# Kernel tuning notes

Measured on AMD Instinct MI355X. Metric: run time of the kernel, lower is better.

The kernel has to match this reference:

```python
import jax, jax.numpy as jnp
import numpy as np
import math

EMBED_DIM = 1024
NUM_HEADS = 16
HEAD_DIM = EMBED_DIM // NUM_HEADS
SEQ = 1024
BATCH = 8


def setup_inputs() -> dict:
    key = jax.random.key(0)
    k1, k2, k3, k4, k5 = jax.random.split(key, 5)
    q = jax.random.normal(k1, (SEQ, BATCH, EMBED_DIM), dtype=jnp.float32)
    # module asserts key == query (self-attention only)
    in_proj_w = jax.random.normal(k2, (3 * EMBED_DIM, EMBED_DIM), dtype=jnp.float32) * 0.02
    in_proj_b = jax.random.normal(k3, (3 * EMBED_DIM,), dtype=jnp.float32) * 0.02
    out_proj_w = jax.random.normal(k4, (EMBED_DIM, EMBED_DIM), dtype=jnp.float32) * 0.02
    out_proj_b = jax.random.normal(k5, (EMBED_DIM,), dtype=jnp.float32) * 0.02
    return {
        "query": q,
        "key": q,
        "value": q,
        "in_proj_w": in_proj_w,
        "in_proj_b": in_proj_b,
        "out_proj_w": out_proj_w,
        "out_proj_b": out_proj_b,
    }


def reference(query, key, value, in_proj_w, in_proj_b, out_proj_w, out_proj_b):
    s, b, e = query.shape
    nh, hd = NUM_HEADS, HEAD_DIM
    norm = math.sqrt(hd)
    # fused QKV projection: [s, b, 3e]
    mixed = query @ in_proj_w.T + in_proj_b
    mixed = mixed.reshape(s, b, nh, 3 * hd)
    q, k, v = jnp.split(mixed, 3, axis=-1)  # each [s, b, nh, hd]
    # -> [b*nh, s, hd]
    q = q.reshape(s, b * nh, hd).transpose(1, 0, 2) / norm
    k = k.reshape(s, b * nh, hd).transpose(1, 0, 2)
    v = v.reshape(s, b * nh, hd).transpose(1, 0, 2)
    # full O(s^2) attention matrix, as in the original bmm/softmax/bmm
    scores = jnp.einsum('nqd,nkd->nqk', q, k)  # [b*nh, s, s]
    probs = jax.nn.softmax(scores, axis=-1)
    ctx = jnp.einsum('nqk,nkd->nqd', probs, v)  # [b*nh, s, hd]
    # [b*nh, s, hd] -> [s, b, e]
    ctx = ctx.reshape(b, nh, s, hd).transpose(2, 0, 1, 3).reshape(s, b, e)
    return ctx @ out_proj_w.T + out_proj_b
```

## Files before the change

### kernel.cpp

```cpp
#include <hip/hip_runtime.h>

typedef __bf16 bf16_t;
typedef __bf16 bf16x8 __attribute__((ext_vector_type(8)));
typedef float f32x4 __attribute__((ext_vector_type(4)));

#define MFMA16(a, b, c) __builtin_amdgcn_mfma_f32_16x16x32_bf16((a), (b), (c), 0, 0, 0)

__device__ __forceinline__ const bf16_t* tile_ptr(const bf16_t* t, int row, int kchunk) {
    return t + row * 64 + (((kchunk ^ (row & 7))) << 3);
}

__device__ __forceinline__ void stage64(const bf16_t* __restrict__ gbase, size_t gstride,
                                        bf16_t* lds_rowbase, int lane) {
    const int rr = lane >> 3, cl = lane & 7;
    const bf16_t* g = gbase + (size_t)rr * gstride + ((cl ^ rr) << 3);
    __builtin_amdgcn_global_load_lds((__attribute__((address_space(1))) const void*)g,
                                     (__attribute__((address_space(3))) void*)lds_rowbase,
                                     16, 0, 0);
}

__global__ void __launch_bounds__(256) k_cvt(
    const float* __restrict__ q, const float* __restrict__ wi, const float* __restrict__ wo,
    bf16_t* __restrict__ qb, bf16_t* __restrict__ wib, bf16_t* __restrict__ wob)
{
    const int g = blockIdx.x * 256 + threadIdx.x;
    const float* src; bf16_t* dst; int off;
    if (g < 1048576)      { src = q;  dst = qb;  off = g; }
    else if (g < 1441792) { src = wi; dst = wib; off = g - 1048576; }
    else                  { src = wo; dst = wob; off = g - 1441792; }
    const float4* s4 = (const float4*)(src + (size_t)off * 8);
    float4 a = s4[0], b = s4[1];
    bf16x8 v;
    v[0] = (bf16_t)a.x; v[1] = (bf16_t)a.y; v[2] = (bf16_t)a.z; v[3] = (bf16_t)a.w;
    v[4] = (bf16_t)b.x; v[5] = (bf16_t)b.y; v[6] = (bf16_t)b.z; v[7] = (bf16_t)b.w;
    *(bf16x8*)(dst + (size_t)off * 8) = v;
}

__global__ void __launch_bounds__(256) k_qkv(
    const bf16_t* __restrict__ A, const bf16_t* __restrict__ W,
    const float* __restrict__ bias,
    bf16_t* __restrict__ Qh, bf16_t* __restrict__ Kh, bf16_t* __restrict__ Vt)
{
    __shared__ bf16_t As[128 * 64];
    __shared__ bf16_t Bs[128 * 64];
    const int m0 = blockIdx.x * 128;
    const int n0 = blockIdx.y * 128;
    const int t = threadIdx.x;
    const int wave = t >> 6, lane = t & 63;
    const int quad = lane >> 4, l16 = lane & 15;
    const int wm = (wave & 1) * 64, wn = (wave >> 1) * 64;

    f32x4 acc[4][4] = {};

    for (int k0 = 0; k0 < 1024; k0 += 64) {
        __syncthreads();
        #pragma unroll
        for (int p = 0; p < 4; ++p) {
            const int rb = wave * 32 + p * 8;
            stage64(A + (size_t)(m0 + rb) * 1024 + k0, 1024, As + rb * 64, lane);
            stage64(W + (size_t)(n0 + rb) * 1024 + k0, 1024, Bs + rb * 64, lane);
        }
        __syncthreads();
        #pragma unroll
        for (int ks = 0; ks < 2; ++ks) {
            bf16x8 af[4], bf[4];
            #pragma unroll
            for (int i = 0; i < 4; ++i)
                af[i] = *(const bf16x8*)tile_ptr(As, wm + i * 16 + l16, ks * 4 + quad);
            #pragma unroll
            for (int j = 0; j < 4; ++j)
                bf[j] = *(const bf16x8*)tile_ptr(Bs, wn + j * 16 + l16, ks * 4 + quad);
            #pragma unroll
            for (int i = 0; i < 4; ++i)
                #pragma unroll
                for (int j = 0; j < 4; ++j)
                    acc[i][j] = MFMA16(af[i], bf[j], acc[i][j]);
        }
    }

    #pragma unroll
    for (int j = 0; j < 4; ++j) {
        const int n = n0 + wn + j * 16 + l16;
        const int h = n / 192;
        const int c = n - h * 192;
        const float bv = bias[n];
        #pragma unroll
        for (int i = 0; i < 4; ++i) {
            #pragma unroll
            for (int rg = 0; rg < 4; ++rg) {
                const int m = m0 + wm + i * 16 + quad * 4 + rg;
                const int si = m >> 3, bi = m & 7;
                const int head = bi * 16 + h;
                const float val = acc[i][j][rg] + bv;
                if (c < 64)
                    Qh[((size_t)head * 1024 + si) * 64 + c] = (bf16_t)(val * 0.125f);
                else if (c < 128)
                    Kh[((size_t)head * 1024 + si) * 64 + (c - 64)] = (bf16_t)val;
                else
                    Vt[((size_t)head * 64 + (c - 128)) * 1024 + si] = (bf16_t)val;
            }
        }
    }
}

__global__ void __launch_bounds__(256) k_attn(
    const bf16_t* __restrict__ Qh, const bf16_t* __restrict__ Kh,
    const bf16_t* __restrict__ Vg, bf16_t* __restrict__ Ctx)
{
    __shared__ bf16_t Qs[128 * 64];
    __shared__ bf16_t Ks[64 * 64];
    __shared__ bf16_t Vts[80 * 64];
    __shared__ bf16_t Ps[4][32][72];

    const int head = blockIdx.x >> 3;
    const int qt = blockIdx.x & 7;
    const int t = threadIdx.x;
    const int wave = t >> 6, lane = t & 63;
    const int quad = lane >> 4, l16 = lane & 15;

    const bf16_t* Qg = Qh + (size_t)head * 65536 + (size_t)qt * 8192;
    const bf16_t* Kg = Kh + (size_t)head * 65536;
    const bf16_t* Vgh = Vg + (size_t)head * 65536;

    #pragma unroll
    for (int p = 0; p < 4; ++p) {
        const int rb = wave * 32 + p * 8;
        stage64(Qg + (size_t)rb * 64, 64, Qs + rb * 64, lane);
    }
    #pragma unroll
    for (int i = 0; i < 4; ++i) {
        const int idx = t * 4 + i;
        Vts[64 * 64 + idx] = (bf16_t)((idx < 64) ? 1.0f : 0.0f);
    }
    __syncthreads();

    bf16x8 qf[2][2];
    #pragma unroll
    for (int half = 0; half < 2; ++half)
        #pragma unroll
        for (int ks = 0; ks < 2; ++ks)
            qf[half][ks] = *(const bf16x8*)tile_ptr(Qs, wave * 32 + half * 16 + l16, ks * 4 + quad);

    f32x4 vacc[2][5] = {};

    for (int kt = 0; kt < 16; ++kt) {
        __syncthreads();
        #pragma unroll
        for (int p = 0; p < 2; ++p) {
            const int rb = wave * 16 + p * 8;
            stage64(Kg + (size_t)(kt * 64 + rb) * 64, 64, Ks + rb * 64, lane);
            stage64(Vgh + (size_t)rb * 1024 + kt * 64, 1024, Vts + rb * 64, lane);
        }
        __syncthreads();

        f32x4 s[2][4] = {};
        #pragma unroll
        for (int ks = 0; ks < 2; ++ks) {
            #pragma unroll
            for (int j = 0; j < 4; ++j) {
                bf16x8 kf = *(const bf16x8*)tile_ptr(Ks, j * 16 + l16, ks * 4 + quad);
                s[0][j] = MFMA16(qf[0][ks], kf, s[0][j]);
                s[1][j] = MFMA16(qf[1][ks], kf, s[1][j]);
            }
        }

        #pragma unroll
        for (int half = 0; half < 2; ++half)
            #pragma unroll
            for (int j = 0; j < 4; ++j)
                #pragma unroll
                for (int rg = 0; rg < 4; ++rg)
                    Ps[wave][half * 16 + quad * 4 + rg][j * 16 + l16] =
                        (bf16_t)exp2f(s[half][j][rg] * 1.44269504088896f);
        asm volatile("s_waitcnt lgkmcnt(0)" ::: "memory");

        #pragma unroll
        for (int ks = 0; ks < 2; ++ks) {
            bf16x8 pf0 = *(const bf16x8*)&Ps[wave][l16][ks * 32 + quad * 8];
            bf16x8 pf1 = *(const bf16x8*)&Ps[wave][16 + l16][ks * 32 + quad * 8];
            #pragma unroll
            for (int n = 0; n < 5; ++n) {
                bf16x8 vf = *(const bf16x8*)tile_ptr(Vts, n * 16 + l16, ks * 4 + quad);
                vacc[0][n] = MFMA16(pf0, vf, vacc[0][n]);
                vacc[1][n] = MFMA16(pf1, vf, vacc[1][n]);
            }
        }
    }

    const int bi = head >> 4, h = head & 15;
    #pragma unroll
    for (int half = 0; half < 2; ++half) {
        #pragma unroll
        for (int rg = 0; rg < 4; ++rg) {
            const float l = __shfl(vacc[half][4][rg], lane & 48, 64);
            const float inv = 1.0f / l;
            const int si = qt * 128 + wave * 32 + half * 16 + quad * 4 + rg;
            #pragma unroll
            for (int n = 0; n < 4; ++n)
                Ctx[((size_t)si * 8 + bi) * 1024 + h * 64 + n * 16 + l16] =
                    (bf16_t)(vacc[half][n][rg] * inv);
        }
    }
}

__global__ void __launch_bounds__(256) k_out(
    const bf16_t* __restrict__ A, const bf16_t* __restrict__ W,
    const float* __restrict__ bias, float* __restrict__ out)
{
    __shared__ bf16_t As[128 * 64];
    __shared__ bf16_t Bs[128 * 64];
    const int m0 = blockIdx.x * 128;
    const int n0 = blockIdx.y * 128;
    const int t = threadIdx.x;
    const int wave = t >> 6, lane = t & 63;
    const int quad = lane >> 4, l16 = lane & 15;
    const int wm = (wave & 1) * 64, wn = (wave >> 1) * 64;

    f32x4 acc[4][4] = {};

    for (int k0 = 0; k0 < 1024; k0 += 64) {
        __syncthreads();
        #pragma unroll
        for (int p = 0; p < 4; ++p) {
            const int rb = wave * 32 + p * 8;
            stage64(A + (size_t)(m0 + rb) * 1024 + k0, 1024, As + rb * 64, lane);
            stage64(W + (size_t)(n0 + rb) * 1024 + k0, 1024, Bs + rb * 64, lane);
        }
        __syncthreads();
        #pragma unroll
        for (int ks = 0; ks < 2; ++ks) {
            bf16x8 af[4], bf[4];
            #pragma unroll
            for (int i = 0; i < 4; ++i)
                af[i] = *(const bf16x8*)tile_ptr(As, wm + i * 16 + l16, ks * 4 + quad);
            #pragma unroll
            for (int j = 0; j < 4; ++j)
                bf[j] = *(const bf16x8*)tile_ptr(Bs, wn + j * 16 + l16, ks * 4 + quad);
            #pragma unroll
            for (int i = 0; i < 4; ++i)
                #pragma unroll
                for (int j = 0; j < 4; ++j)
                    acc[i][j] = MFMA16(af[i], bf[j], acc[i][j]);
        }
    }

    #pragma unroll
    for (int j = 0; j < 4; ++j) {
        const int n = n0 + wn + j * 16 + l16;
        const float bv = bias[n];
        #pragma unroll
        for (int i = 0; i < 4; ++i) {
            #pragma unroll
            for (int rg = 0; rg < 4; ++rg) {
                const int m = m0 + wm + i * 16 + quad * 4 + rg;
                out[(size_t)m * 1024 + n] = acc[i][j][rg] + bv;
            }
        }
    }
}

extern "C" void kernel_launch(void* const* d_in, const int* in_sizes, int n_in,
                              void* d_out, int out_size, void* d_ws, size_t ws_size,
                              hipStream_t stream)
{
    const float* query = (const float*)d_in[0];
    const float* in_w  = (const float*)d_in[3];
    const float* in_b  = (const float*)d_in[4];
    const float* out_w = (const float*)d_in[5];
    const float* out_b = (const float*)d_in[6];
    float* out = (float*)d_out;

    bf16_t* Wi  = (bf16_t*)d_ws;
    bf16_t* Wo  = Wi + (size_t)3145728;
    bf16_t* Qh  = Wo + (size_t)1048576;
    bf16_t* Kh  = Qh + (size_t)8388608;
    bf16_t* Vt  = Kh + (size_t)8388608;
    bf16_t* Aq  = Vt + (size_t)8388608;
    bf16_t* Ctx = Aq;

    k_cvt<<<dim3(6144), 256, 0, stream>>>(query, in_w, out_w, Aq, Wi, Wo);
    k_qkv<<<dim3(64, 24), 256, 0, stream>>>(Aq, Wi, in_b, Qh, Kh, Vt);
    k_attn<<<dim3(1024), 256, 0, stream>>>(Qh, Kh, Vt, Ctx);
    k_out<<<dim3(64, 8), 256, 0, stream>>>(Ctx, Wo, out_b, out);
}
```

Baseline: 317.3 us.

## Stage QKV epilogue through LDS for coalesced stores and blocked V layout

The QKV GEMM now permutes weight rows so each 128-wide output tile is all Q, all K, or all V for two heads. The epilogue writes results into swizzled shared memory, then emits 16-byte coalesced stores instead of scattered 2-byte writes. V is stored in a blocked layout of 8-sequence chunks that the attention kernel loads directly. The attention kernel also keeps the ones column for the row-sum MFMA in registers instead of reading it from LDS. This adds an extra LDS round trip and index arithmetic in the epilogue.

```diff
diff --git a/kernel.cpp b/kernel.cpp
--- a/kernel.cpp
+++ b/kernel.cpp
@@ -17,6 +17,10 @@
     __builtin_amdgcn_global_load_lds((__attribute__((address_space(1))) const void*)g,
                                      (__attribute__((address_space(3))) void*)lds_rowbase,
                                      16, 0, 0);
+}
+
+__device__ __forceinline__ int cs_addr(int m, int n) {
+    return m * 128 + ((((n >> 3) ^ ((m >> 3) & 7))) << 3) + (n & 7);
 }
 
 __global__ void __launch_bounds__(256) k_cvt(
@@ -41,6 +45,221 @@
     const float* __restrict__ bias,
     bf16_t* __restrict__ Qh, bf16_t* __restrict__ Kh, bf16_t* __restrict__ Vt)
 {
+    __shared__ bf16_t smem[16384];
+    bf16_t* As = smem;
+    bf16_t* Bs = smem + 8192;
+    const int m0 = blockIdx.x * 128;
+    const int n0 = blockIdx.y * 128;
+    const int which = n0 >> 10;
+    const int hbase = (n0 & 1023) >> 6;
+    const int t = threadIdx.x;
+    const int wave = t >> 6, lane = t & 63;
+    const int quad = lane >> 4, l16 = lane & 15;
+    const int wm = (wave & 1) * 64, wn = (wave >> 1) * 64;
+
+    f32x4 acc[4][4] = {};
+
+    for (int k0 = 0; k0 < 1024; k0 += 64) {
+        __syncthreads();
+        #pragma unroll
+        for (int p = 0; p < 4; ++p) {
+            const int rb = wave * 32 + p * 8;
+            stage64(A + (size_t)(m0 + rb) * 1024 + k0, 1024, As + rb * 64, lane);
+            const int np = n0 + rb;
+            const int wrow = ((np & 1023) >> 6) * 192 + which * 64 + (np & 63);
+            stage64(W + (size_t)wrow * 1024 + k0, 1024, Bs + rb * 64, lane);
+        }
+        __syncthreads();
+        #pragma unroll
+        for (int ks = 0; ks < 2; ++ks) {
+            bf16x8 af[4], bf[4];
+            #pragma unroll
+            for (int i = 0; i < 4; ++i)
+                af[i] = *(const bf16x8*)tile_ptr(As, wm + i * 16 + l16, ks * 4 + quad);
+            #pragma unroll
+            for (int j = 0; j < 4; ++j)
+                bf[j] = *(const bf16x8*)tile_ptr(Bs, wn + j * 16 + l16, ks * 4 + quad);
+            #pragma unroll
+            for (int i = 0; i < 4; ++i)
+                #pragma unroll
+                for (int j = 0; j < 4; ++j)
+                    acc[i][j] = MFMA16(af[i], bf[j], acc[i][j]);
+        }
+    }
+
+    __syncthreads();
+    const float scale = (which == 0) ? 0.125f : 1.0f;
+    #pragma unroll
+    for (int j = 0; j < 4; ++j) {
+        const int nl = wn + j * 16 + l16;
+        const float bv = bias[(hbase + (nl >> 6)) * 192 + which * 64 + (nl & 63)];
+        #pragma unroll
+        for (int i = 0; i < 4; ++i) {
+            #pragma unroll
+            for (int rg = 0; rg < 4; ++rg) {
+                const int ml = wm + i * 16 + quad * 4 + rg;
+                smem[cs_addr(ml, nl)] = (bf16_t)((acc[i][j][rg] + bv) * scale);
+            }
+        }
+    }
+    __syncthreads();
+
+    const int si0 = m0 >> 3;
+    if (which < 2) {
+        bf16_t* dst = which ? Kh : Qh;
+        #pragma unroll
+        for (int u = 0; u < 4; ++u) {
+            const int unit = wave * 4 + u;
+            const int h = unit >> 3, bi = unit & 7;
+            const int head = bi * 16 + hbase + h;
+            #pragma unroll
+            for (int pass = 0; pass < 2; ++pass) {
+                const int si = pass * 8 + (lane >> 3);
+                const int dc = lane & 7;
+                const int ml = si * 8 + bi;
+                const int nch = (h * 8 + dc) ^ (si & 7);
+                bf16x8 v = *(const bf16x8*)&smem[ml * 128 + nch * 8];
+                *(bf16x8*)(dst + (size_t)head * 65536 + (size_t)(si0 + si) * 64 + dc * 8) = v;
+            }
+        }
+    } else {
+        #pragma unroll
+        for (int u = 0; u < 8; ++u) {
+            const int unit = wave * 8 + u;
+            const int h = unit >> 4, bi = (unit >> 1) & 7, c = unit & 1;
+            const int head = bi * 16 + hbase + h;
+            const int d = lane;
+            bf16x8 v;
+            #pragma unroll
+            for (int e = 0; e < 8; ++e) {
+                const int ml = (c * 8 + e) * 8 + bi;
+                const int nch = (h * 8 + (d >> 3)) ^ e;
+                v[e] = smem[ml * 128 + nch * 8 + (d & 7)];
+            }
+            *(bf16x8*)(Vt + (size_t)head * 65536 +
+                       (size_t)(si0 / 8 + c) * 512 + (size_t)d * 8) = v;
+        }
+    }
+}
+
+__global__ void __launch_bounds__(256) k_attn(
+    const bf16_t* __restrict__ Qh, const bf16_t* __restrict__ Kh,
+    const bf16_t* __restrict__ Vg, bf16_t* __restrict__ Ctx)
+{
+    __shared__ bf16_t Qs[128 * 64];
+    __shared__ bf16_t Ks[64 * 64];
+    __shared__ bf16_t Vts[80 * 64];
+    __shared__ bf16_t Ps[4][32][72];
+
+    const int head = blockIdx.x >> 3;
+    const int qt = blockIdx.x & 7;
+    const int t = threadIdx.x;
+    const int wave = t >> 6, lane = t & 63;
+    const int quad = lane >> 4, l16 = lane & 15;
+
+    const bf16_t* Qg = Qh + (size_t)head * 65536 + (size_t)qt * 8192;
+    const bf16_t* Kg = Kh + (size_t)head * 65536;
+    const bf16_t* Vgh = Vg + (size_t)head * 65536;
+
+    #pragma unroll
+    for (int p = 0; p < 4; ++p) {
+        const int rb = wave * 32 + p * 8;
+        stage64(Qg + (size_t)rb * 64, 64, Qs + rb * 64, lane);
+    }
+    #pragma unroll
+    for (int i = 0; i < 4; ++i) {
+        const int idx = t * 4 + i;
+        Vts[64 * 64 + idx] = (bf16_t)((idx < 64) ? 1.0f : 0.0f);
+    }
+    __syncthreads();
+
+    bf16x8 qf[2][2];
+    #pragma unroll
+    for (int half = 0; half < 2; ++half)
+        #pragma unroll
+        for (int ks = 0; ks < 2; ++ks)
+            qf[half][ks] = *(const bf16x8*)tile_ptr(Qs, wave * 32 + half * 16 + l16, ks * 4 + quad);
+
+    bf16x8 vf_ones[2];
+    #pragma unroll
+    for (int ks = 0; ks < 2; ++ks)
+        vf_ones[ks] = *(const bf16x8*)tile_ptr(Vts, 64 + l16, ks * 4 + quad);
+
+    f32x4 vacc[2][5] = {};
+
+    for (int kt = 0; kt < 16; ++kt) {
+        __syncthreads();
+        #pragma unroll
+        for (int p = 0; p < 2; ++p) {
+            const int rb = wave * 16 + p * 8;
+            stage64(Kg + (size_t)(kt * 64 + rb) * 64, 64, Ks + rb * 64, lane);
+            {
+                const int rr = lane >> 3, cl = lane & 7;
+                const bf16_t* g = Vgh + (size_t)(kt * 8 + (cl ^ rr)) * 512
+                                      + (size_t)(rb + rr) * 8;
+                __builtin_amdgcn_global_load_lds(
+                    (__attribute__((address_space(1))) const void*)g,
+                    (__attribute__((address_space(3))) void*)(Vts + rb * 64), 16, 0, 0);
+            }
+        }
+        __syncthreads();
+
+        f32x4 s[2][4] = {};
+        #pragma unroll
+        for (int ks = 0; ks < 2; ++ks) {
+            #pragma unroll
+            for (int j = 0; j < 4; ++j) {
+                bf16x8 kf = *(const bf16x8*)tile_ptr(Ks, j * 16 + l16, ks * 4 + quad);
+                s[0][j] = MFMA16(qf[0][ks], kf, s[0][j]);
+                s[1][j] = MFMA16(qf[1][ks], kf, s[1][j]);
+            }
+        }
+
+        #pragma unroll
+        for (int half = 0; half < 2; ++half)
+            #pragma unroll
+            for (int j = 0; j < 4; ++j)
+                #pragma unroll
+                for (int rg = 0; rg < 4; ++rg)
+                    Ps[wave][half * 16 + quad * 4 + rg][j * 16 + l16] =
+                        (bf16_t)exp2f(s[half][j][rg] * 1.44269504088896f);
+        asm volatile("s_waitcnt lgkmcnt(0)" ::: "memory");
+
+        #pragma unroll
+        for (int ks = 0; ks < 2; ++ks) {
+            bf16x8 pf0 = *(const bf16x8*)&Ps[wave][l16][ks * 32 + quad * 8];
+            bf16x8 pf1 = *(const bf16x8*)&Ps[wave][16 + l16][ks * 32 + quad * 8];
+            #pragma unroll
+            for (int n = 0; n < 4; ++n) {
+                bf16x8 vf = *(const bf16x8*)tile_ptr(Vts, n * 16 + l16, ks * 4 + quad);
+                vacc[0][n] = MFMA16(pf0, vf, vacc[0][n]);
+                vacc[1][n] = MFMA16(pf1, vf, vacc[1][n]);
+            }
+            vacc[0][4] = MFMA16(pf0, vf_ones[ks], vacc[0][4]);
+            vacc[1][4] = MFMA16(pf1, vf_ones[ks], vacc[1][4]);
+        }
+    }
+
+    const int bi = head >> 4, h = head & 15;
+    #pragma unroll
+    for (int half = 0; half < 2; ++half) {
+        #pragma unroll
+        for (int rg = 0; rg < 4; ++rg) {
+            const float l = __shfl(vacc[half][4][rg], lane & 48, 64);
+            const float inv = 1.0f / l;
+            const int si = qt * 128 + wave * 32 + half * 16 + quad * 4 + rg;
+            #pragma unroll
+            for (int n = 0; n < 4; ++n)
+                Ctx[((size_t)si * 8 + bi) * 1024 + h * 64 + n * 16 + l16] =
+                    (bf16_t)(vacc[half][n][rg] * inv);
+        }
+    }
+}
+
+__global__ void __launch_bounds__(256) k_out(
+    const bf16_t* __restrict__ A, const bf16_t* __restrict__ W,
+    const float* __restrict__ bias, float* __restrict__ out)
+{
     __shared__ bf16_t As[128 * 64];
     __shared__ bf16_t Bs[128 * 64];
     const int m0 = blockIdx.x * 128;
@@ -81,172 +300,6 @@
     #pragma unroll
     for (int j = 0; j < 4; ++j) {
         const int n = n0 + wn + j * 16 + l16;
-        const int h = n / 192;
-        const int c = n - h * 192;
-        const float bv = bias[n];
-        #pragma unroll
-        for (int i = 0; i < 4; ++i) {
-            #pragma unroll
-            for (int rg = 0; rg < 4; ++rg) {
-                const int m = m0 + wm + i * 16 + quad * 4 + rg;
-                const int si = m >> 3, bi = m & 7;
-                const int head = bi * 16 + h;
-                const float val = acc[i][j][rg] + bv;
-                if (c < 64)
-                    Qh[((size_t)head * 1024 + si) * 64 + c] = (bf16_t)(val * 0.125f);
-                else if (c < 128)
-                    Kh[((size_t)head * 1024 + si) * 64 + (c - 64)] = (bf16_t)val;
-                else
-                    Vt[((size_t)head * 64 + (c - 128)) * 1024 + si] = (bf16_t)val;
-            }
-        }
-    }
-}
-
-__global__ void __launch_bounds__(256) k_attn(
-    const bf16_t* __restrict__ Qh, const bf16_t* __restrict__ Kh,
-    const bf16_t* __restrict__ Vg, bf16_t* __restrict__ Ctx)
-{
-    __shared__ bf16_t Qs[128 * 64];
-    __shared__ bf16_t Ks[64 * 64];
-    __shared__ bf16_t Vts[80 * 64];
-    __shared__ bf16_t Ps[4][32][72];
-
-    const int head = blockIdx.x >> 3;
-    const int qt = blockIdx.x & 7;
-    const int t = threadIdx.x;
-    const int wave = t >> 6, lane = t & 63;
-    const int quad = lane >> 4, l16 = lane & 15;
-
-    const bf16_t* Qg = Qh + (size_t)head * 65536 + (size_t)qt * 8192;
-    const bf16_t* Kg = Kh + (size_t)head * 65536;
-    const bf16_t* Vgh = Vg + (size_t)head * 65536;
-
-    #pragma unroll
-    for (int p = 0; p < 4; ++p) {
-        const int rb = wave * 32 + p * 8;
-        stage64(Qg + (size_t)rb * 64, 64, Qs + rb * 64, lane);
-    }
-    #pragma unroll
-    for (int i = 0; i < 4; ++i) {
-        const int idx = t * 4 + i;
-        Vts[64 * 64 + idx] = (bf16_t)((idx < 64) ? 1.0f : 0.0f);
-    }
-    __syncthreads();
-
-    bf16x8 qf[2][2];
-    #pragma unroll
-    for (int half = 0; half < 2; ++half)
-        #pragma unroll
-        for (int ks = 0; ks < 2; ++ks)
-            qf[half][ks] = *(const bf16x8*)tile_ptr(Qs, wave * 32 + half * 16 + l16, ks * 4 + quad);
-
-    f32x4 vacc[2][5] = {};
-
-    for (int kt = 0; kt < 16; ++kt) {
-        __syncthreads();
-        #pragma unroll
-        for (int p = 0; p < 2; ++p) {
-            const int rb = wave * 16 + p * 8;
-            stage64(Kg + (size_t)(kt * 64 + rb) * 64, 64, Ks + rb * 64, lane);
-            stage64(Vgh + (size_t)rb * 1024 + kt * 64, 1024, Vts + rb * 64, lane);
-        }
-        __syncthreads();
-
-        f32x4 s[2][4] = {};
-        #pragma unroll
-        for (int ks = 0; ks < 2; ++ks) {
-            #pragma unroll
-            for (int j = 0; j < 4; ++j) {
-                bf16x8 kf = *(const bf16x8*)tile_ptr(Ks, j * 16 + l16, ks * 4 + quad);
-                s[0][j] = MFMA16(qf[0][ks], kf, s[0][j]);
-                s[1][j] = MFMA16(qf[1][ks], kf, s[1][j]);
-            }
-        }
-
-        #pragma unroll
-        for (int half = 0; half < 2; ++half)
-            #pragma unroll
-            for (int j = 0; j < 4; ++j)
-                #pragma unroll
-                for (int rg = 0; rg < 4; ++rg)
-                    Ps[wave][half * 16 + quad * 4 + rg][j * 16 + l16] =
-                        (bf16_t)exp2f(s[half][j][rg] * 1.44269504088896f);
-        asm volatile("s_waitcnt lgkmcnt(0)" ::: "memory");
-
-        #pragma unroll
-        for (int ks = 0; ks < 2; ++ks) {
-            bf16x8 pf0 = *(const bf16x8*)&Ps[wave][l16][ks * 32 + quad * 8];
-            bf16x8 pf1 = *(const bf16x8*)&Ps[wave][16 + l16][ks * 32 + quad * 8];
-            #pragma unroll
-            for (int n = 0; n < 5; ++n) {
-                bf16x8 vf = *(const bf16x8*)tile_ptr(Vts, n * 16 + l16, ks * 4 + quad);
-                vacc[0][n] = MFMA16(pf0, vf, vacc[0][n]);
-                vacc[1][n] = MFMA16(pf1, vf, vacc[1][n]);
-            }
-        }
-    }
-
-    const int bi = head >> 4, h = head & 15;
-    #pragma unroll
-    for (int half = 0; half < 2; ++half) {
-        #pragma unroll
-        for (int rg = 0; rg < 4; ++rg) {
-            const float l = __shfl(vacc[half][4][rg], lane & 48, 64);
-            const float inv = 1.0f / l;
-            const int si = qt * 128 + wave * 32 + half * 16 + quad * 4 + rg;
-            #pragma unroll
-            for (int n = 0; n < 4; ++n)
-                Ctx[((size_t)si * 8 + bi) * 1024 + h * 64 + n * 16 + l16] =
-                    (bf16_t)(vacc[half][n][rg] * inv);
-        }
-    }
-}
-
-__global__ void __launch_bounds__(256) k_out(
-    const bf16_t* __restrict__ A, const bf16_t* __restrict__ W,
-    const float* __restrict__ bias, float* __restrict__ out)
-{
-    __shared__ bf16_t As[128 * 64];
-    __shared__ bf16_t Bs[128 * 64];
-    const int m0 = blockIdx.x * 128;
-    const int n0 = blockIdx.y * 128;
-    const int t = threadIdx.x;
-    const int wave = t >> 6, lane = t & 63;
-    const int quad = lane >> 4, l16 = lane & 15;
-    const int wm = (wave & 1) * 64, wn = (wave >> 1) * 64;
-
-    f32x4 acc[4][4] = {};
-
-    for (int k0 = 0; k0 < 1024; k0 += 64) {
-        __syncthreads();
-        #pragma unroll
-        for (int p = 0; p < 4; ++p) {
-            const int rb = wave * 32 + p * 8;
-            stage64(A + (size_t)(m0 + rb) * 1024 + k0, 1024, As + rb * 64, lane);
-            stage64(W + (size_t)(n0 + rb) * 1024 + k0, 1024, Bs + rb * 64, lane);
-        }
-        __syncthreads();
-        #pragma unroll
-        for (int ks = 0; ks < 2; ++ks) {
-            bf16x8 af[4], bf[4];
-            #pragma unroll
-            for (int i = 0; i < 4; ++i)
-                af[i] = *(const bf16x8*)tile_ptr(As, wm + i * 16 + l16, ks * 4 + quad);
-            #pragma unroll
-            for (int j = 0; j < 4; ++j)
-                bf[j] = *(const bf16x8*)tile_ptr(Bs, wn + j * 16 + l16, ks * 4 + quad);
-            #pragma unroll
-            for (int i = 0; i < 4; ++i)
-                #pragma unroll
-                for (int j = 0; j < 4; ++j)
-                    acc[i][j] = MFMA16(af[i], bf[j], acc[i][j]);
-        }
-    }
-
-    #pragma unroll
-    for (int j = 0; j < 4; ++j) {
-        const int n = n0 + wn + j * 16 + l16;
         const float bv = bias[n];
         #pragma unroll
         for (int i = 0; i < 4; ++i) {
```

New measurement: 310.0 us. 1.02x faster.
